# Kernel tuning notes

Measured on AMD Instinct MI355X. Metric: run time of the kernel, lower is better.

Reference implementation:

```python
import jax, jax.numpy as jnp
import numpy as np

B, S, E, H, K, V = 2, 2048, 2048, 16, 128, 128
EPS = 1e-5


def _rotate(x, cos, sin):
    half = K // 2
    swapped = jnp.concatenate((x[..., half:], x[..., :half]), axis=-1)
    return cos * x + sin * swapped


def setup_inputs() -> dict:
    key = jax.random.key(0)
    k1, k2, k3 = jax.random.split(key, 3)
    embeddings = jax.random.normal(k1, (B, S, E), jnp.float32)
    pos = jnp.arange(S, dtype=jnp.float32)[:, None]
    inv_freq = 1.0 / (10000.0 ** (jnp.arange(0, K, 2, dtype=jnp.float32) / K))
    ang = pos * inv_freq[None, :]
    ang = jnp.concatenate((ang, ang), axis=-1)
    cosb = jnp.cos(ang)[None, None, :, :]
    sinb = jnp.sin(ang)[None, None, :, :]
    cos_buffer = jnp.stack((cosb, cosb))
    sin_buffer = jnp.stack((sinb, sinb))
    causal_buffer = jnp.tril(jnp.ones((S, S), dtype=bool))[None, None]
    w_norm = jnp.ones((E,), jnp.float32)
    w_qkv = jax.random.normal(k2, (E, 2 * K * H + V * H), jnp.float32) * 0.02
    w_out = jax.random.normal(k3, (H * V, E), jnp.float32) * 0.02
    return dict(embeddings=embeddings, cos_buffer=cos_buffer, sin_buffer=sin_buffer,
                causal_buffer=causal_buffer, w_norm=w_norm, w_qkv=w_qkv, w_out=w_out)


def reference(embeddings, cos_buffer, sin_buffer, causal_buffer, w_norm, w_qkv, w_out):
    ms = jnp.mean(embeddings * embeddings, axis=-1, keepdims=True)
    normed = embeddings * jax.lax.rsqrt(ms + EPS) * w_norm
    qkv = normed @ w_qkv
    ks = K * H
    q = qkv[..., :ks].reshape(B, S, H, K).transpose(0, 2, 1, 3)
    k = qkv[..., ks:2 * ks].reshape(B, S, H, K).transpose(0, 2, 1, 3)
    v = qkv[..., 2 * ks:].reshape(B, S, H, V).transpose(0, 2, 1, 3)
    present_k, present_v = k, v
    q = _rotate(q, cos_buffer[0], sin_buffer[0])
    k = _rotate(k, cos_buffer[1], sin_buffer[1])
    scores = jnp.einsum('bhqk,bhsk->bhqs', q, k) / np.float32(np.sqrt(K))
    scores = jnp.where(causal_buffer, scores, -jnp.inf)
    attn = jax.nn.softmax(scores, axis=-1)
    out = jnp.einsum('bhqs,bhsv->bhqv', attn, v)
    out = out.transpose(0, 2, 1, 3).reshape(B, S, H * V) @ w_out
    return embeddings + out, present_k, present_v
```

## Files before the change

kernel.cpp:

```cpp
#include <hip/hip_runtime.h>

typedef unsigned short u16;
typedef unsigned int   u32;
typedef short bf16x8 __attribute__((ext_vector_type(8)));
typedef float f32x4  __attribute__((ext_vector_type(4)));
typedef float f4     __attribute__((ext_vector_type(4)));
typedef u16   u16x4  __attribute__((ext_vector_type(4)));
typedef u16   u16x8  __attribute__((ext_vector_type(8)));
typedef u32   u32x2  __attribute__((ext_vector_type(2)));

__device__ __forceinline__ u16 f2bf(float x) {
  u32 u = __float_as_uint(x);
  u += 0x7fff + ((u >> 16) & 1);
  return (u16)(u >> 16);
}
__device__ __forceinline__ float bf2f(u16 h) {
  return __uint_as_float(((u32)h) << 16);
}
__device__ __forceinline__ void gload16(const void* g, void* l) {
  __builtin_amdgcn_global_load_lds((const __attribute__((address_space(1))) u32*)g,
                                   (__attribute__((address_space(3))) u32*)l, 16, 0, 0);
}
__device__ __forceinline__ f32x4 mfma16(bf16x8 a, bf16x8 b, f32x4 c) {
  return __builtin_amdgcn_mfma_f32_16x16x32_bf16(a, b, c, 0, 0, 0);
}

__global__ __launch_bounds__(256) void k_rmsnorm(const float* __restrict__ x,
                                                 const float* __restrict__ w,
                                                 u16* __restrict__ out) {
  const int row = blockIdx.x, tid = threadIdx.x;
  const float* xr = x + (size_t)row * 2048;
  f4 a = *(const f4*)&xr[tid * 8];
  f4 b = *(const f4*)&xr[tid * 8 + 4];
  float ss = a[0]*a[0]+a[1]*a[1]+a[2]*a[2]+a[3]*a[3]+b[0]*b[0]+b[1]*b[1]+b[2]*b[2]+b[3]*b[3];
#pragma unroll
  for (int off = 32; off > 0; off >>= 1) ss += __shfl_xor(ss, off);
  __shared__ float red[4];
  if ((tid & 63) == 0) red[tid >> 6] = ss;
  __syncthreads();
  ss = red[0] + red[1] + red[2] + red[3];
  const float sc = rsqrtf(ss * (1.0f / 2048.0f) + 1e-5f);
  f4 wa = *(const f4*)&w[tid * 8];
  f4 wb = *(const f4*)&w[tid * 8 + 4];
  u16x8 o;
#pragma unroll
  for (int i = 0; i < 4; ++i) o[i] = f2bf(a[i] * sc * wa[i]);
#pragma unroll
  for (int i = 0; i < 4; ++i) o[4 + i] = f2bf(b[i] * sc * wb[i]);
  *(u16x8*)&out[(size_t)row * 2048 + tid * 8] = o;
}

__global__ __launch_bounds__(256) void k_transpose_cvt(const float* __restrict__ src,
                                                       u16* __restrict__ dst,
                                                       int R, int C) {
  __shared__ float t[32][33];
  const int tid = threadIdx.x;
  const size_t zoff = (size_t)blockIdx.z * (size_t)R * (size_t)C;
  src += zoff; dst += zoff;
  const int r0 = blockIdx.y * 32, c0 = blockIdx.x * 32;
  const int rr = tid >> 3, cc = (tid & 7) * 4;
  f4 v = *(const f4*)&src[(size_t)(r0 + rr) * C + c0 + cc];
  t[rr][cc] = v[0]; t[rr][cc + 1] = v[1]; t[rr][cc + 2] = v[2]; t[rr][cc + 3] = v[3];
  __syncthreads();
  const int oc = tid >> 3, orr = (tid & 7) * 4;
  u16x4 o;
#pragma unroll
  for (int k = 0; k < 4; ++k) o[k] = f2bf(t[orr + k][oc]);
  *(u16x4*)&dst[(size_t)(c0 + oc) * R + r0 + orr] = o;
}

template <int EPI>
__global__ __launch_bounds__(256) void k_gemm128(
    const u16* __restrict__ A, const u16* __restrict__ Bt,
    u16* __restrict__ q_pre, float* __restrict__ outK, float* __restrict__ outV,
    const float* __restrict__ emb, float* __restrict__ out0,
    u16* __restrict__ vtf) {
  constexpr int KD = 2048;
  __shared__ __align__(16) u16 lA[128 * 64];
  __shared__ __align__(16) u16 lB[128 * 64];
  const int tid = threadIdx.x;
  const int lane = tid & 63;
  const int w = tid >> 6;
  const int wr = w >> 1, wc = w & 1;
  const int g = lane >> 4, c15 = lane & 15;
  const int m0 = blockIdx.y * 128, n0 = blockIdx.x * 128;
  f32x4 acc[4][4] = {};
  for (int kt = 0; kt < KD / 64; ++kt) {
    __syncthreads();
#pragma unroll
    for (int p = 0; p < 4; ++p) {
      int c = p * 256 + tid;
      int row = c >> 3, ch = c & 7;
      int gch = ch ^ (row & 7);
      gload16(&A[(size_t)(m0 + row) * KD + kt * 64 + gch * 8], &lA[c * 8]);
      gload16(&Bt[(size_t)(n0 + row) * KD + kt * 64 + gch * 8], &lB[c * 8]);
    }
    __syncthreads();
#pragma unroll
    for (int ks = 0; ks < 2; ++ks) {
      bf16x8 af[4], bfr[4];
#pragma unroll
      for (int i = 0; i < 4; ++i) {
        int row = wr * 64 + i * 16 + c15;
        int chn = (ks * 4 + g) ^ (row & 7);
        af[i] = *(const bf16x8*)&lA[row * 64 + chn * 8];
      }
#pragma unroll
      for (int j = 0; j < 4; ++j) {
        int row = wc * 64 + j * 16 + c15;
        int chn = (ks * 4 + g) ^ (row & 7);
        bfr[j] = *(const bf16x8*)&lB[row * 64 + chn * 8];
      }
#pragma unroll
      for (int i = 0; i < 4; ++i)
#pragma unroll
        for (int j = 0; j < 4; ++j)
          acc[i][j] = mfma16(af[i], bfr[j], acc[i][j]);
    }
  }
  const int rb = m0 + wr * 64 + g * 4;
  const int cb = wc * 64 + c15;
  if (EPI == 0) {
    const int sec = n0 >> 11;
    const int h = (n0 & 2047) >> 7;
#pragma unroll
    for (int i = 0; i < 4; ++i)
#pragma unroll
      for (int j = 0; j < 4; ++j) {
        const int d = cb + j * 16;
        const int mb = rb + i * 16;
        const int b_ = mb >> 11, s0 = mb & 2047;
#pragma unroll
        for (int r = 0; r < 4; ++r) {
          size_t o = ((size_t)(b_ * 16 + h) * 2048 + (s0 + r)) * 128 + d;
          float val = acc[i][j][r];
          if (sec == 0)      q_pre[o] = f2bf(val);
          else if (sec == 1) outK[o] = val;
          else               outV[o] = val;
        }
        if (sec == 2 && vtf != nullptr) {
          u16x4 vt;
#pragma unroll
          for (int r = 0; r < 4; ++r) vt[r] = f2bf(acc[i][j][r]);
          *(u16x4*)&vtf[((size_t)(b_ * 16 + h) * 128 + d) * 2048 + s0] = vt;
        }
      }
  } else {
#pragma unroll
    for (int i = 0; i < 4; ++i)
#pragma unroll
      for (int j = 0; j < 4; ++j)
#pragma unroll
        for (int r = 0; r < 4; ++r) {
          int mm = rb + i * 16 + r;
          int nn = n0 + cb + j * 16;
          size_t o = (size_t)mm * 2048 + nn;
          out0[o] = acc[i][j][r] + emb[o];
        }
  }
}

__global__ __launch_bounds__(256) void k_rope(const u16* __restrict__ qp,
                                              const float* __restrict__ kp,
                                              const float* __restrict__ cosb,
                                              const float* __restrict__ sinb,
                                              u16* __restrict__ qr, u16* __restrict__ kr) {
  const int gid = blockIdx.x * 256 + threadIdx.x;
  const int row = gid >> 4;
  const int d0 = (gid & 15) * 4;
  const int s = row & 2047;
  const float SC = 0.08838834764831845f;
  const float* c1 = cosb + (size_t)s * 128;
  const float* s1 = sinb + (size_t)s * 128;
  const float* c2 = c1 + 262144;
  const float* s2 = s1 + 262144;
  const size_t base = (size_t)row * 128;
  f4 cl = *(const f4*)&c1[d0], ch = *(const f4*)&c1[d0 + 64];
  f4 sl = *(const f4*)&s1[d0], sh = *(const f4*)&s1[d0 + 64];
  {
    u16x4 xl = *(const u16x4*)&qp[base + d0];
    u16x4 xh = *(const u16x4*)&qp[base + d0 + 64];
    u16x4 ol, oh;
#pragma unroll
    for (int i = 0; i < 4; ++i) {
      float lo = bf2f(xl[i]), hi = bf2f(xh[i]);
      ol[i] = f2bf((cl[i] * lo + sl[i] * hi) * SC);
      oh[i] = f2bf((ch[i] * hi + sh[i] * lo) * SC);
    }
    *(u16x4*)&qr[base + d0] = ol;
    *(u16x4*)&qr[base + d0 + 64] = oh;
  }
  {
    f4 c2l = *(const f4*)&c2[d0], c2h = *(const f4*)&c2[d0 + 64];
    f4 s2l = *(const f4*)&s2[d0], s2h = *(const f4*)&s2[d0 + 64];
    f4 xl = *(const f4*)&kp[base + d0];
    f4 xh = *(const f4*)&kp[base + d0 + 64];
    u16x4 ol, oh;
#pragma unroll
    for (int i = 0; i < 4; ++i) {
      ol[i] = f2bf(c2l[i] * xl[i] + s2l[i] * xh[i]);
      oh[i] = f2bf(c2h[i] * xh[i] + s2h[i] * xl[i]);
    }
    *(u16x4*)&kr[base + d0] = ol;
    *(u16x4*)&kr[base + d0 + 64] = oh;
  }
}

__device__ __forceinline__ void stage_kv(const u16* kb, const u16* vb, int kv0,
                                         u16* dK, u16* dV, int tid) {
#pragma unroll
  for (int p = 0; p < 4; ++p) {
    int c = p * 256 + tid;
    { int row = c >> 4, ch = c & 15, gch = ch ^ (row & 7);
      gload16(&kb[(size_t)(kv0 + row) * 128 + gch * 8], &dK[c * 8]); }
    { int row = c >> 3, ch = c & 7, gch = ch ^ (row & 7);
      gload16(&vb[(size_t)row * 2048 + kv0 + gch * 8], &dV[c * 8]); }
  }
}

__global__ __launch_bounds__(256) void k_attn(const u16* __restrict__ q_rot,
                                              const u16* __restrict__ k_rot,
                                              const u16* __restrict__ v_t,
                                              u16* __restrict__ attn_o) {
  const int bh = blockIdx.y;
  const int b = bh >> 4, h = bh & 15;
  const int tid = threadIdx.x, w = tid >> 6, lane = tid & 63;
  const int g = lane >> 4, c15 = lane & 15;
  __shared__ __align__(16) u16 lK[2][64 * 128];
  __shared__ __align__(16) u16 lV[2][128 * 64];
  __shared__ __align__(16) u16 lP[4][16 * 64];

  const u16* qb = q_rot + (size_t)bh * 2048 * 128;
  const u16* kb = k_rot + (size_t)bh * 2048 * 128;
  const u16* vb = v_t + (size_t)bh * 128 * 2048;
  const float L2E = 1.442695040888963f;
  const float SHIFT = 11.541560327111707f;

  for (int halfp = 0; halfp < 2; ++halfp) {
    const int qt = halfp ? (int)blockIdx.x : 31 - (int)blockIdx.x;
    const int q0 = qt * 64;
    const int nt = qt + 1;

    bf16x8 qf[4];
    const int qrow = q0 + w * 16 + c15;
#pragma unroll
    for (int f = 0; f < 4; ++f)
      qf[f] = *(const bf16x8*)&qb[(size_t)qrow * 128 + f * 32 + g * 8];

    f32x4 O[8];
#pragma unroll
    for (int i = 0; i < 8; ++i) O[i] = {0.f, 0.f, 0.f, 0.f};
    float lsum = 0.0f;

    stage_kv(kb, vb, 0, &lK[0][0], &lV[0][0], tid);
    asm volatile("s_waitcnt vmcnt(0)" ::: "memory");
    __builtin_amdgcn_s_barrier();

    int cur = 0;
    for (int t = 0; t < nt; ++t) {
      if (t + 1 < nt)
        stage_kv(kb, vb, (t + 1) * 64, &lK[cur ^ 1][0], &lV[cur ^ 1][0], tid);

      const int kv0 = t * 64;
      f32x4 S[4];
#pragma unroll
      for (int n = 0; n < 4; ++n) S[n] = {0.f, 0.f, 0.f, 0.f};
      __builtin_amdgcn_s_setprio(1);
#pragma unroll
      for (int ks = 0; ks < 4; ++ks) {
#pragma unroll
        for (int n = 0; n < 4; ++n) {
          int row = n * 16 + c15;
          int chn = (ks * 4 + g) ^ (row & 7);
          bf16x8 kf = *(const bf16x8*)&lK[cur][row * 128 + chn * 8];
          S[n] = mfma16(kf, qf[ks], S[n]);
        }
      }
      __builtin_amdgcn_s_setprio(0);

      if (t == nt - 1) {
#pragma unroll
        for (int n = 0; n < 4; ++n)
#pragma unroll
          for (int r = 0; r < 4; ++r)
            if (kv0 + n * 16 + g * 4 + r > qrow) S[n][r] = -1e30f;
      }
#pragma unroll
      for (int n = 0; n < 4; ++n) {
        float p0 = exp2f(__builtin_fmaf(S[n][0], L2E, -SHIFT));
        float p1 = exp2f(__builtin_fmaf(S[n][1], L2E, -SHIFT));
        float p2 = exp2f(__builtin_fmaf(S[n][2], L2E, -SHIFT));
        float p3 = exp2f(__builtin_fmaf(S[n][3], L2E, -SHIFT));
        lsum += (p0 + p1) + (p2 + p3);
        u32x2 pw;
        pw[0] = (u32)f2bf(p0) | ((u32)f2bf(p1) << 16);
        pw[1] = (u32)f2bf(p2) | ((u32)f2bf(p3) << 16);
        int chunk = n * 2 + (g >> 1);
        int eoff = c15 * 64 + ((chunk ^ (c15 & 7)) << 3) + ((g & 1) << 2);
        *(u32x2*)&lP[w][eoff] = pw;
      }

      __builtin_amdgcn_s_setprio(1);
#pragma unroll
      for (int ks = 0; ks < 2; ++ks) {
        int ch2 = (ks * 4 + g) ^ (c15 & 7);
        bf16x8 pf = *(const bf16x8*)&lP[w][c15 * 64 + ch2 * 8];
#pragma unroll
        for (int nn = 0; nn < 8; ++nn) {
          int row = nn * 16 + c15;
          int chn = (ks * 4 + g) ^ (row & 7);
          bf16x8 vf = *(const bf16x8*)&lV[cur][row * 64 + chn * 8];
          O[nn] = mfma16(pf, vf, O[nn]);
        }
      }
      __builtin_amdgcn_s_setprio(0);

      asm volatile("s_waitcnt vmcnt(0)" ::: "memory");
      __builtin_amdgcn_s_barrier();
      cur ^= 1;
    }

    lsum += __shfl_xor(lsum, 16);
    lsum += __shfl_xor(lsum, 32);
    const float inv = 1.0f / lsum;
    float invr[4];
#pragma unroll
    for (int r = 0; r < 4; ++r)
      invr[r] = __shfl(inv, g * 4 + r);
#pragma unroll
    for (int nn = 0; nn < 8; ++nn)
#pragma unroll
      for (int r = 0; r < 4; ++r) {
        int s_ = q0 + w * 16 + g * 4 + r;
        int col = h * 128 + nn * 16 + c15;
        attn_o[(size_t)(b * 2048 + s_) * 2048 + col] = f2bf(O[nn][r] * invr[r]);
      }
  }
}

extern "C" void kernel_launch(void* const* d_in, const int* in_sizes, int n_in,
                              void* d_out, int out_size, void* d_ws, size_t ws_size,
                              hipStream_t stream) {
  const float* emb    = (const float*)d_in[0];
  const float* cosb   = (const float*)d_in[1];
  const float* sinb   = (const float*)d_in[2];
  const float* w_norm = (const float*)d_in[4];
  const float* w_qkv  = (const float*)d_in[5];
  const float* w_out  = (const float*)d_in[6];

  float* out0 = (float*)d_out;
  float* outK = out0 + 8388608;
  float* outV = out0 + 16777216;

  char* ws = (char*)d_ws;
  u16* normed = (u16*)(ws + 0);
  u16* wqkvT  = (u16*)(ws + 16777216);
  u16* woutT  = (u16*)(ws + 41943040);
  u16* q_pre  = (u16*)(ws + 50331648);
  u16* q_rot  = (u16*)(ws + 67108864);
  u16* k_rot  = (u16*)(ws + 83886080);
  u16* attn_o = normed;

  const bool fuse_vt = ws_size >= (size_t)117440512;
  u16* v_t = fuse_vt ? (u16*)(ws + 100663296) : wqkvT;

  k_rmsnorm<<<4096, 256, 0, stream>>>(emb, w_norm, normed);
  k_transpose_cvt<<<dim3(192, 64, 1), 256, 0, stream>>>(w_qkv, wqkvT, 2048, 6144);
  k_transpose_cvt<<<dim3(64, 64, 1), 256, 0, stream>>>(w_out, woutT, 2048, 2048);
  k_gemm128<0><<<dim3(48, 32), 256, 0, stream>>>(normed, wqkvT, q_pre, outK, outV,
                                                 nullptr, nullptr,
                                                 fuse_vt ? v_t : nullptr);
  k_rope<<<4096, 256, 0, stream>>>(q_pre, outK, cosb, sinb, q_rot, k_rot);
  if (!fuse_vt)
    k_transpose_cvt<<<dim3(4, 64, 32), 256, 0, stream>>>(outV, v_t, 2048, 128);
  k_attn<<<dim3(16, 32), 256, 0, stream>>>(q_rot, k_rot, v_t, attn_o);
  k_gemm128<1><<<dim3(16, 32), 256, 0, stream>>>(attn_o, woutT, nullptr, nullptr, nullptr,
                                                 emb, out0, nullptr);
}
```

Measured before the change: 304.7 us.

## Double-buffer LDS tiles in 128x128 GEMM to overlap global loads with MFMA

Converts the GEMM main loop to a two-stage LDS ping-pong: the next K tile is issued via global_load_lds into the alternate buffer while MFMAs run on the current one, with one waitcnt+barrier per iteration instead of two syncthreads. It also raises wave priority around the MFMA block with s_setprio. LDS use doubles to 64KB per block, which may reduce occupancy.

```diff
diff --git a/kernel.cpp b/kernel.cpp
--- a/kernel.cpp
+++ b/kernel.cpp
@@ -69,15 +69,28 @@
   *(u16x4*)&dst[(size_t)(c0 + oc) * R + r0 + orr] = o;
 }
 
+__device__ __forceinline__ void stage128(const u16* __restrict__ A,
+                                         const u16* __restrict__ Bt,
+                                         int m0, int n0, int kt,
+                                         u16* dA, u16* dB, int tid) {
+#pragma unroll
+  for (int p = 0; p < 4; ++p) {
+    int c = p * 256 + tid;
+    int row = c >> 3, ch = c & 7, gch = ch ^ (row & 7);
+    gload16(&A[(size_t)(m0 + row) * 2048 + kt * 64 + gch * 8], &dA[c * 8]);
+    gload16(&Bt[(size_t)(n0 + row) * 2048 + kt * 64 + gch * 8], &dB[c * 8]);
+  }
+}
+
 template <int EPI>
 __global__ __launch_bounds__(256) void k_gemm128(
     const u16* __restrict__ A, const u16* __restrict__ Bt,
     u16* __restrict__ q_pre, float* __restrict__ outK, float* __restrict__ outV,
     const float* __restrict__ emb, float* __restrict__ out0,
     u16* __restrict__ vtf) {
-  constexpr int KD = 2048;
-  __shared__ __align__(16) u16 lA[128 * 64];
-  __shared__ __align__(16) u16 lB[128 * 64];
+  constexpr int NT = 32;
+  __shared__ __align__(16) u16 lA[2][128 * 64];
+  __shared__ __align__(16) u16 lB[2][128 * 64];
   const int tid = threadIdx.x;
   const int lane = tid & 63;
   const int w = tid >> 6;
@@ -85,17 +98,16 @@
   const int g = lane >> 4, c15 = lane & 15;
   const int m0 = blockIdx.y * 128, n0 = blockIdx.x * 128;
   f32x4 acc[4][4] = {};
-  for (int kt = 0; kt < KD / 64; ++kt) {
-    __syncthreads();
-#pragma unroll
-    for (int p = 0; p < 4; ++p) {
-      int c = p * 256 + tid;
-      int row = c >> 3, ch = c & 7;
-      int gch = ch ^ (row & 7);
-      gload16(&A[(size_t)(m0 + row) * KD + kt * 64 + gch * 8], &lA[c * 8]);
-      gload16(&Bt[(size_t)(n0 + row) * KD + kt * 64 + gch * 8], &lB[c * 8]);
-    }
-    __syncthreads();
+
+  stage128(A, Bt, m0, n0, 0, lA[0], lB[0], tid);
+  asm volatile("s_waitcnt vmcnt(0)" ::: "memory");
+  __builtin_amdgcn_s_barrier();
+
+  for (int kt = 0; kt < NT; ++kt) {
+    const int cur = kt & 1;
+    if (kt + 1 < NT)
+      stage128(A, Bt, m0, n0, kt + 1, lA[cur ^ 1], lB[cur ^ 1], tid);
+
 #pragma unroll
     for (int ks = 0; ks < 2; ++ks) {
       bf16x8 af[4], bfr[4];
@@ -103,21 +115,26 @@
       for (int i = 0; i < 4; ++i) {
         int row = wr * 64 + i * 16 + c15;
         int chn = (ks * 4 + g) ^ (row & 7);
-        af[i] = *(const bf16x8*)&lA[row * 64 + chn * 8];
+        af[i] = *(const bf16x8*)&lA[cur][row * 64 + chn * 8];
       }
 #pragma unroll
       for (int j = 0; j < 4; ++j) {
         int row = wc * 64 + j * 16 + c15;
         int chn = (ks * 4 + g) ^ (row & 7);
-        bfr[j] = *(const bf16x8*)&lB[row * 64 + chn * 8];
-      }
+        bfr[j] = *(const bf16x8*)&lB[cur][row * 64 + chn * 8];
+      }
+      __builtin_amdgcn_s_setprio(1);
 #pragma unroll
       for (int i = 0; i < 4; ++i)
 #pragma unroll
         for (int j = 0; j < 4; ++j)
           acc[i][j] = mfma16(af[i], bfr[j], acc[i][j]);
+      __builtin_amdgcn_s_setprio(0);
     }
-  }
+    asm volatile("s_waitcnt vmcnt(0)" ::: "memory");
+    __builtin_amdgcn_s_barrier();
+  }
+
   const int rb = m0 + wr * 64 + g * 4;
   const int cb = wc * 64 + c15;
   if (EPI == 0) {
```

Measured after the change: 298.0 us. -2.2%, faster.
